# Performance work log

Hardware: AMD Instinct MI355X
Metric: run time of the kernel (lower is better)

The kernel has to match this reference:

```python
import jax, jax.numpy as jnp
import numpy as np


def setup_inputs() -> dict:
    key = jax.random.key(0)
    ks = jax.random.split(key, 5)
    B, C, H, W = 4, 512, 64, 64
    A = 64  # attention_features
    s = lambda fan_in: 1.0 / np.sqrt(fan_in)
    return {
        "x": jax.random.normal(ks[0], (B, C, H, W), dtype=jnp.float32),
        "Wf": jax.random.normal(ks[1], (C, A), dtype=jnp.float32) * s(C),
        "bf": jnp.zeros((A,), dtype=jnp.float32),
        "Wg": jax.random.normal(ks[2], (C, A), dtype=jnp.float32) * s(C),
        "bg": jnp.zeros((A,), dtype=jnp.float32),
        "Wh": jax.random.normal(ks[3], (C, C), dtype=jnp.float32) * s(C),
        "bh": jnp.zeros((C,), dtype=jnp.float32),
        "scale": jax.random.uniform(ks[4], (), dtype=jnp.float32),
    }


def reference(x, Wf, bf, Wg, bg, Wh, bh, scale):
    B, C, H, W = x.shape
    N = H * W

    def conv1x1(w, b):  # 1x1 conv == per-pixel matmul over channels
        return jnp.einsum('bchw,cf->bfhw', x, w) + b[None, :, None, None]

    f = conv1x1(Wf, bf)  # [B, A, H, W]
    g = conv1x1(Wg, bg)  # [B, A, H, W]
    h = conv1x1(Wh, bh)  # [B, C, H, W]

    # flatten_hw (channels_first): [B, C', H, W] -> [B, N, C']
    flat = lambda t: t.reshape(B, t.shape[1], N).transpose(0, 2, 1)
    gf = flat(g)  # [B, N, A]
    ff = flat(f)  # [B, N, A]
    hf = flat(h)  # [B, N, C]

    s = jnp.einsum('bnd,bmd->bnm', gf, ff)       # [B, N, N]
    attn = jax.nn.softmax(s, axis=-1)
    o = jnp.einsum('bnm,bmc->bnc', attn, hf)     # [B, N, C]
    # Original does a raw reshape back to x's shape (no transpose) — keep it.
    y = scale * o.reshape(x.shape) + x
    return y
```

## Files before the change

kernel.cpp:

```cpp
#include <hip/hip_runtime.h>
#include <hip/hip_bf16.h>

constexpr int BB = 4;
constexpr int C  = 512;
constexpr int A  = 64;
constexpr int N  = 4096;

typedef __attribute__((ext_vector_type(8))) short s16x8;
typedef __attribute__((ext_vector_type(4))) float f32x4;

#define MFMA_16x16x32_BF16(a, b, c) __builtin_amdgcn_mfma_f32_16x16x32_bf16((a), (b), (c), 0, 0, 0)

typedef __attribute__((address_space(3))) unsigned int lds_u32_t;
typedef const __attribute__((address_space(1))) unsigned int glb_u32_t;

__device__ __forceinline__ void gl2lds16(const void* g, void* l) {
    __builtin_amdgcn_global_load_lds((glb_u32_t*)g, (lds_u32_t*)l, 16, 0, 0);
}

#define GLOAD(dst, base, off)                                                  \
    asm volatile("global_load_dwordx4 %0, %1, %2"                              \
                 : "=v"(dst) : "v"(off), "s"(base))

__global__ __launch_bounds__(256) void k_trans(const float* __restrict__ src,
                                               __hip_bfloat16* __restrict__ dst,
                                               int K, int M) {
    __shared__ __hip_bfloat16 Ls[64][66];
    int m0 = blockIdx.x << 6, k0 = blockIdx.y << 6;
    size_t bo = (size_t)blockIdx.z * K * M;
    int t = threadIdx.x;
    int lm = t & 63, g = t >> 6;
    #pragma unroll
    for (int j = 0; j < 16; ++j) {
        int kk = j * 4 + g;
        Ls[kk][lm] = __float2bfloat16(src[bo + (size_t)(k0 + kk) * M + m0 + lm]);
    }
    __syncthreads();
    #pragma unroll
    for (int j = 0; j < 16; ++j) {
        int mm = j * 4 + g;
        dst[bo + (size_t)(m0 + mm) * K + k0 + lm] = Ls[lm][mm];
    }
}

__global__ __launch_bounds__(256) void k_trans2(const float* __restrict__ src,
                                                __hip_bfloat16* __restrict__ dhi,
                                                __hip_bfloat16* __restrict__ dlo,
                                                int K, int M) {
    __shared__ float Ls[64][65];
    int m0 = blockIdx.x << 6, k0 = blockIdx.y << 6;
    size_t bo = (size_t)blockIdx.z * K * M;
    int t = threadIdx.x;
    int lm = t & 63, g = t >> 6;
    #pragma unroll
    for (int j = 0; j < 16; ++j) {
        int kk = j * 4 + g;
        Ls[kk][lm] = src[bo + (size_t)(k0 + kk) * M + m0 + lm];
    }
    __syncthreads();
    #pragma unroll
    for (int j = 0; j < 16; ++j) {
        int mm = j * 4 + g;
        float v = Ls[lm][mm];
        __hip_bfloat16 h = __float2bfloat16(v);
        size_t idx = bo + (size_t)(m0 + mm) * K + k0 + lm;
        dhi[idx] = h;
        dlo[idx] = __float2bfloat16(v - __bfloat162float(h));
    }
}

__global__ __launch_bounds__(256) void k_fgm(const __hip_bfloat16* __restrict__ XThi, const __hip_bfloat16* __restrict__ XTlo,
                                             const __hip_bfloat16* __restrict__ WfThi, const __hip_bfloat16* __restrict__ WfTlo,
                                             const __hip_bfloat16* __restrict__ WgThi, const __hip_bfloat16* __restrict__ WgTlo,
                                             const float* __restrict__ bfv, const float* __restrict__ bgv,
                                             __hip_bfloat16* __restrict__ FFhi, __hip_bfloat16* __restrict__ FFlo,
                                             __hip_bfloat16* __restrict__ GFhi, __hip_bfloat16* __restrict__ GFlo) {
    __shared__ __align__(16) __hip_bfloat16 Ah[64 * 32], Al[64 * 32];
    __shared__ __align__(16) __hip_bfloat16 Bh[128 * 32], Bl[128 * 32];
    int r0 = blockIdx.x << 6;
    int t = threadIdx.x;
    int w = t >> 6, l = t & 63;
    int ln15 = l & 15, quad = l >> 4;
    int mh = w & 1, nh = w >> 1;

    f32x4 acc[2][4];
    #pragma unroll
    for (int mi = 0; mi < 2; ++mi)
        #pragma unroll
        for (int ni = 0; ni < 4; ++ni) acc[mi][ni] = (f32x4){0.f, 0.f, 0.f, 0.f};

    for (int kt = 0; kt < C; kt += 32) {
        {
            int row = t >> 2, seg = t & 3;
            int gseg = (seg - (row >> 1)) & 3;
            size_t go = (size_t)(r0 + row) * C + kt + gseg * 8;
            gl2lds16(XThi + go, &Ah[t * 8]);
            gl2lds16(XTlo + go, &Al[t * 8]);
        }
        #pragma unroll
        for (int j = 0; j < 2; ++j) {
            int i = j * 256 + t;
            int row = i >> 2, seg = i & 3;
            int gseg = (seg - (row >> 1)) & 3;
            size_t go = (size_t)(row & 63) * C + kt + gseg * 8;
            const __hip_bfloat16* bh = j ? WgThi : WfThi;
            const __hip_bfloat16* bl = j ? WgTlo : WfTlo;
            gl2lds16(bh + go, &Bh[i * 8]);
            gl2lds16(bl + go, &Bl[i * 8]);
        }
        __syncthreads();
        s16x8 afh[2], afl[2], bfh[4], bfl[4];
        #pragma unroll
        for (int mi = 0; mi < 2; ++mi) {
            int row = mh * 32 + mi * 16 + ln15;
            int sw = ((quad + (row >> 1)) & 3) << 3;
            afh[mi] = *(const s16x8*)&Ah[row * 32 + sw];
            afl[mi] = *(const s16x8*)&Al[row * 32 + sw];
        }
        #pragma unroll
        for (int ni = 0; ni < 4; ++ni) {
            int row = nh * 64 + ni * 16 + ln15;
            int sw = ((quad + (row >> 1)) & 3) << 3;
            bfh[ni] = *(const s16x8*)&Bh[row * 32 + sw];
            bfl[ni] = *(const s16x8*)&Bl[row * 32 + sw];
        }
        #pragma unroll
        for (int mi = 0; mi < 2; ++mi)
            #pragma unroll
            for (int ni = 0; ni < 4; ++ni) {
                acc[mi][ni] = MFMA_16x16x32_BF16(afh[mi], bfh[ni], acc[mi][ni]);
                acc[mi][ni] = MFMA_16x16x32_BF16(afl[mi], bfh[ni], acc[mi][ni]);
                acc[mi][ni] = MFMA_16x16x32_BF16(afh[mi], bfl[ni], acc[mi][ni]);
            }
        __syncthreads();
    }

    #pragma unroll
    for (int mi = 0; mi < 2; ++mi) {
        #pragma unroll
        for (int r = 0; r < 4; ++r) {
            size_t grow = (size_t)(r0 + mh * 32 + mi * 16 + quad * 4 + r) * A;
            #pragma unroll
            for (int ni = 0; ni < 4; ++ni) {
                int col = nh * 64 + ni * 16 + ln15;
                if (col < A) {
                    float v = acc[mi][ni][r] + bfv[col];
                    __hip_bfloat16 h = __float2bfloat16(v);
                    FFhi[grow + col] = h;
                    FFlo[grow + col] = __float2bfloat16(v - __bfloat162float(h));
                } else {
                    int a = col - A;
                    float v = acc[mi][ni][r] + bgv[a];
                    __hip_bfloat16 h = __float2bfloat16(v);
                    GFhi[grow + a] = h;
                    GFlo[grow + a] = __float2bfloat16(v - __bfloat162float(h));
                }
            }
        }
    }
}

__global__ __launch_bounds__(256) void k_hm(const __hip_bfloat16* __restrict__ WhT,
                                            const __hip_bfloat16* __restrict__ XT,
                                            const float* __restrict__ bhv,
                                            __hip_bfloat16* __restrict__ HFT) {
    __shared__ __align__(16) __hip_bfloat16 As[128 * 32];
    __shared__ __align__(16) __hip_bfloat16 Bs[128 * 32];
    int b  = blockIdx.z;
    int c0 = blockIdx.x << 7;
    int n0 = blockIdx.y << 7;
    int t = threadIdx.x;
    int w = t >> 6, l = t & 63;
    int ln15 = l & 15, quad = l >> 4;
    int mc = (w >> 1) << 6, nn = (w & 1) << 6;

    const __hip_bfloat16* Bb = XT + (size_t)b * N * C;

    f32x4 acc[4][4];
    #pragma unroll
    for (int mi = 0; mi < 4; ++mi)
        #pragma unroll
        for (int ni = 0; ni < 4; ++ni) acc[mi][ni] = (f32x4){0.f, 0.f, 0.f, 0.f};

    for (int kt = 0; kt < C; kt += 32) {
        #pragma unroll
        for (int j = 0; j < 2; ++j) {
            int i = j * 256 + t;
            int row = i >> 2, seg = i & 3;
            int gseg = (seg - (row >> 1)) & 3;
            gl2lds16(WhT + ((size_t)(c0 + row) * C + kt + gseg * 8), &As[i * 8]);
        }
        #pragma unroll
        for (int j = 0; j < 2; ++j) {
            int i = j * 256 + t;
            int row = i >> 2, seg = i & 3;
            int gseg = (seg - (row >> 1)) & 3;
            gl2lds16(Bb + ((size_t)(n0 + row) * C + kt + gseg * 8), &Bs[i * 8]);
        }
        __syncthreads();
        s16x8 af[4], bf2[4];
        #pragma unroll
        for (int mi = 0; mi < 4; ++mi) {
            int row = mc + mi * 16 + ln15;
            int sw = ((quad + (row >> 1)) & 3) << 3;
            af[mi] = *(const s16x8*)&As[row * 32 + sw];
        }
        #pragma unroll
        for (int ni = 0; ni < 4; ++ni) {
            int row = nn + ni * 16 + ln15;
            int sw = ((quad + (row >> 1)) & 3) << 3;
            bf2[ni] = *(const s16x8*)&Bs[row * 32 + sw];
        }
        #pragma unroll
        for (int mi = 0; mi < 4; ++mi)
            #pragma unroll
            for (int ni = 0; ni < 4; ++ni)
                acc[mi][ni] = MFMA_16x16x32_BF16(af[mi], bf2[ni], acc[mi][ni]);
        __syncthreads();
    }

    #pragma unroll
    for (int mi = 0; mi < 4; ++mi) {
        #pragma unroll
        for (int r = 0; r < 4; ++r) {
            int c = c0 + mc + mi * 16 + quad * 4 + r;
            float bias = bhv[c];
            size_t rowbase = ((size_t)b * C + c) * N;
            #pragma unroll
            for (int ni = 0; ni < 4; ++ni) {
                int n = n0 + nn + ni * 16 + ln15;
                HFT[rowbase + n] = __float2bfloat16(acc[mi][ni][r] + bias);
            }
        }
    }
}

__global__ __launch_bounds__(512, 2) void k_so(const __hip_bfloat16* __restrict__ GFhi, const __hip_bfloat16* __restrict__ GFlo,
                                               const __hip_bfloat16* __restrict__ FFhi, const __hip_bfloat16* __restrict__ FFlo,
                                               const __hip_bfloat16* __restrict__ HFT,
                                               const float* __restrict__ x,
                                               const float* __restrict__ scalep,
                                               float* __restrict__ out) {
    __shared__ __align__(16) __hip_bfloat16 Pl[2][64 * 64];
    __shared__ float sred[8][32];
    __shared__ float rsum[64];

    int id  = blockIdx.x;
    int xcd = id & 7;
    int b   = xcd >> 1;
    int qs  = ((id >> 3) << 1) | (xcd & 1);
    int q0  = qs << 6;

    int t = threadIdx.x;
    int w = t >> 6, l = t & 63;
    int ln15 = l & 15, quad = l >> 4, q8 = quad << 3;
    int qh = w >> 2, kq = w & 3;

    const __hip_bfloat16* Fh = FFhi + (size_t)b * N * A;
    const __hip_bfloat16* Fl = FFlo + (size_t)b * N * A;
    const __hip_bfloat16* Hb = HFT  + (size_t)b * C * N;

    s16x8 ah[2][2], al[2][2];
    #pragma unroll
    for (int mi = 0; mi < 2; ++mi) {
        const __hip_bfloat16* gp = GFhi + (size_t)(b * N + q0 + qh * 32 + mi * 16 + ln15) * A + q8;
        const __hip_bfloat16* lp = GFlo + (size_t)(b * N + q0 + qh * 32 + mi * 16 + ln15) * A + q8;
        ah[mi][0] = *(const s16x8*)gp; ah[mi][1] = *(const s16x8*)(gp + 32);
        al[mi][0] = *(const s16x8*)lp; al[mi][1] = *(const s16x8*)(lp + 32);
    }

    f32x4 acc[4][4];
    #pragma unroll
    for (int mi = 0; mi < 4; ++mi)
        #pragma unroll
        for (int ni = 0; ni < 4; ++ni) acc[mi][ni] = (f32x4){0.f, 0.f, 0.f, 0.f};
    float sm[2][4] = {{0.f,0.f,0.f,0.f},{0.f,0.f,0.f,0.f}};

    uint32_t hoffb[4];
    #pragma unroll
    for (int ni = 0; ni < 4; ++ni)
        hoffb[ni] = (uint32_t)((((w * 64 + ni * 16 + ln15) * N) + q8) * 2);
    uint32_t foff = (uint32_t)(((kq * 16 + ln15) * A + q8) * 2);
    int key2 = (kq * 16 + ln15) << 1;

    s16x8 hA[8], hB[8], fA[4], fB[4];
    #pragma unroll
    for (int ni = 0; ni < 4; ++ni) {
        GLOAD(hA[ni],     Hb, hoffb[ni]);
        GLOAD(hA[4 + ni], Hb, hoffb[ni] + 64u);
    }
    GLOAD(fA[0], Fh, foff);
    GLOAD(fA[1], Fh, foff + 64u);
    GLOAD(fA[2], Fl, foff);
    GLOAD(fA[3], Fl, foff + 64u);

#define KITER(KT, PBUF, HC, FC, HN, FN)                                        \
    {                                                                          \
        int ktn = ((KT) + 64) & (N - 1);     \
        uint32_t ktn2 = (uint32_t)(ktn << 1);                                  \
        uint32_t ktnf = (uint32_t)(ktn << 7);                                  \
        _Pragma("unroll")                                                      \
        for (int ni = 0; ni < 4; ++ni) {                                       \
            GLOAD(HN[ni],     Hb, hoffb[ni] + ktn2);                           \
            GLOAD(HN[4 + ni], Hb, hoffb[ni] + ktn2 + 64u);                     \
        }                                                                      \
        GLOAD(FN[0], Fh, foff + ktnf);                                         \
        GLOAD(FN[1], Fh, foff + ktnf + 64u);                                   \
        GLOAD(FN[2], Fl, foff + ktnf);                                         \
        GLOAD(FN[3], Fl, foff + ktnf + 64u);                                   \
        asm volatile("s_waitcnt vmcnt(12)" ::: "memory");                      \
        __builtin_amdgcn_sched_barrier(0);                                     \
        _Pragma("unroll")                                                      \
        for (int mi = 0; mi < 2; ++mi) {                                       \
            f32x4 s = {0.f, 0.f, 0.f, 0.f};                                    \
            s = MFMA_16x16x32_BF16(ah[mi][0], FC[0], s);                       \
            s = MFMA_16x16x32_BF16(ah[mi][1], FC[1], s);                       \
            s = MFMA_16x16x32_BF16(al[mi][0], FC[0], s);                       \
            s = MFMA_16x16x32_BF16(al[mi][1], FC[1], s);                       \
            s = MFMA_16x16x32_BF16(ah[mi][0], FC[2], s);                       \
            s = MFMA_16x16x32_BF16(ah[mi][1], FC[3], s);                       \
            _Pragma("unroll")                                                  \
            for (int r = 0; r < 4; ++r) {                                      \
                int q = qh * 32 + mi * 16 + quad * 4 + r;                      \
                float p = __expf(s[r]);         \
                __hip_bfloat16 pb = __float2bfloat16(p);                       \
                sm[mi][r] += __bfloat162float(pb);                             \
                *(__hip_bfloat16*)((char*)(PBUF) + q * 128 + (key2 ^ ((q & 7) << 4))) = pb; \
            }                                                                  \
        }                                                                      \
        asm volatile("s_waitcnt lgkmcnt(0)" ::: "memory");                     \
        __builtin_amdgcn_sched_barrier(0);                                     \
        __builtin_amdgcn_s_barrier();         \
        _Pragma("unroll")                                                      \
        for (int ks = 0; ks < 2; ++ks) {                                       \
            s16x8 pa[4];                                                       \
            _Pragma("unroll")                                                  \
            for (int mi = 0; mi < 4; ++mi) {                                   \
                int q = mi * 16 + ln15;                                        \
                pa[mi] = *(const s16x8*)((char*)(PBUF) + q * 128 + ((ks * 64 + quad * 16) ^ ((q & 7) << 4))); \
            }                                                                  \
            _Pragma("unroll")                                                  \
            for (int mi = 0; mi < 4; ++mi)                                     \
                _Pragma("unroll")                                              \
                for (int ni = 0; ni < 4; ++ni)                                 \
                    acc[mi][ni] = MFMA_16x16x32_BF16(pa[mi], HC[ks * 4 + ni], acc[mi][ni]); \
        }                                                                      \
    }

    for (int kt = 0; kt < N; kt += 128) {
        KITER(kt,      (&Pl[0][0]), hA, fA, hB, fB);
        KITER(kt + 64, (&Pl[1][0]), hB, fB, hA, fA);
    }
#undef KITER

    #pragma unroll
    for (int mi = 0; mi < 2; ++mi)
        #pragma unroll
        for (int r = 0; r < 4; ++r)
            #pragma unroll
            for (int d = 1; d < 16; d <<= 1)
                sm[mi][r] += __shfl_xor(sm[mi][r], d, 64);
    if (ln15 == 0) {
        #pragma unroll
        for (int mi = 0; mi < 2; ++mi)
            #pragma unroll
            for (int r = 0; r < 4; ++r)
                sred[w][mi * 16 + quad * 4 + r] = sm[mi][r];
    }
    __syncthreads();
    if (t < 64) {
        int base = (t >> 5) << 2, ix = t & 31;
        rsum[t] = sred[base][ix] + sred[base + 1][ix] + sred[base + 2][ix] + sred[base + 3][ix];
    }
    __syncthreads();

    float scv = *scalep;
    #pragma unroll
    for (int mi = 0; mi < 4; ++mi) {
        #pragma unroll
        for (int r = 0; r < 4; ++r) {
            int q = mi * 16 + quad * 4 + r;
            float srs = scv / rsum[q];
            size_t rowbase = (size_t)(b * N + q0 + q) * C;
            #pragma unroll
            for (int ni = 0; ni < 4; ++ni) {
                size_t idx = rowbase + w * 64 + ni * 16 + ln15;
                out[idx] = acc[mi][ni][r] * srs + x[idx];
            }
        }
    }
}

extern "C" void kernel_launch(void* const* d_in, const int* in_sizes, int n_in,
                              void* d_out, int out_size, void* d_ws, size_t ws_size,
                              hipStream_t stream) {
    const float* x   = (const float*)d_in[0];
    const float* Wf  = (const float*)d_in[1];
    const float* bfv = (const float*)d_in[2];
    const float* Wg  = (const float*)d_in[3];
    const float* bgv = (const float*)d_in[4];
    const float* Wh  = (const float*)d_in[5];
    const float* bhv = (const float*)d_in[6];
    const float* sc  = (const float*)d_in[7];
    float* out = (float*)d_out;

    char* ws = (char*)d_ws;
    size_t off = 0;
    __hip_bfloat16* FFhi = (__hip_bfloat16*)(ws + off); off += (size_t)BB * N * A * 2;
    __hip_bfloat16* FFlo = (__hip_bfloat16*)(ws + off); off += (size_t)BB * N * A * 2;
    __hip_bfloat16* GFhi = (__hip_bfloat16*)(ws + off); off += (size_t)BB * N * A * 2;
    __hip_bfloat16* GFlo = (__hip_bfloat16*)(ws + off); off += (size_t)BB * N * A * 2;
    __hip_bfloat16* HFT  = (__hip_bfloat16*)(ws + off); off += (size_t)BB * C * N * 2;
    char* Pbase          = (ws + off);                  off += (size_t)BB * N * N * 2;
    off += (size_t)BB * N * 4;
    __hip_bfloat16* WhT  = (__hip_bfloat16*)(ws + off); off += (size_t)C * C * 2;
    __hip_bfloat16* WfThi = (__hip_bfloat16*)(ws + off); off += (size_t)A * C * 2;
    __hip_bfloat16* WfTlo = (__hip_bfloat16*)(ws + off); off += (size_t)A * C * 2;
    __hip_bfloat16* WgThi = (__hip_bfloat16*)(ws + off); off += (size_t)A * C * 2;
    __hip_bfloat16* WgTlo = (__hip_bfloat16*)(ws + off); off += (size_t)A * C * 2;
    __hip_bfloat16* XThi = (__hip_bfloat16*)(Pbase + (size_t)BB * N * N * 2 - (size_t)BB * N * C * 2);
    __hip_bfloat16* XTlo = (__hip_bfloat16*)(Pbase + (size_t)BB * N * N * 2 - 2 * (size_t)BB * N * C * 2);

    k_trans<<<dim3(C / 64, C / 64, 1), dim3(256), 0, stream>>>(Wh, WhT, C, C);
    k_trans2<<<dim3(N / 64, C / 64, BB), dim3(256), 0, stream>>>(x, XThi, XTlo, C, N);
    k_trans2<<<dim3(A / 64, C / 64, 1), dim3(256), 0, stream>>>(Wf, WfThi, WfTlo, C, A);
    k_trans2<<<dim3(A / 64, C / 64, 1), dim3(256), 0, stream>>>(Wg, WgThi, WgTlo, C, A);
    k_hm<<<dim3(C / 128, N / 128, BB), dim3(256), 0, stream>>>(WhT, XThi, bhv, HFT);
    k_fgm<<<dim3((BB * N) / 64), dim3(256), 0, stream>>>(XThi, XTlo, WfThi, WfTlo, WgThi, WgTlo,
                                                         bfv, bgv, FFhi, FFlo, GFhi, GFlo);
    k_so<<<dim3(BB * (N / 64)), dim3(512), 0, stream>>>(GFhi, GFlo, FFhi, FFlo, HFT, x, sc, out);
}
```

Measured before the change: 346.9 us.

## Stage H tiles into LDS via async global-to-LDS loads with double buffering

The H operand of the attention-times-values MFMA is now loaded from global memory straight into a double-buffered LDS tile with swizzled layout, instead of directly into registers. The P buffer shrinks to a single buffer, with an extra barrier at the end of each iteration to protect it. Wave priority raising (s_setprio) is added around the MFMA sections. This frees VGPRs and may give better-coalesced H loads, but the kernel now needs about 136KB of LDS per block, so two 512-thread blocks can no longer share a CU. It also adds a barrier per iteration.

```diff
diff --git a/kernel.cpp b/kernel.cpp
--- a/kernel.cpp
+++ b/kernel.cpp
@@ -241,7 +241,8 @@
                                                const float* __restrict__ x,
                                                const float* __restrict__ scalep,
                                                float* __restrict__ out) {
-    __shared__ __align__(16) __hip_bfloat16 Pl[2][64 * 64];
+    __shared__ __align__(16) __hip_bfloat16 Hs[2][C * 64];
+    __shared__ __align__(16) __hip_bfloat16 Pl[64 * 64];
     __shared__ float sred[8][32];
     __shared__ float rsum[64];
 
@@ -255,6 +256,7 @@
     int w = t >> 6, l = t & 63;
     int ln15 = l & 15, quad = l >> 4, q8 = quad << 3;
     int qh = w >> 2, kq = w & 3;
+    int lr = l >> 3, ls = l & 7;
 
     const __hip_bfloat16* Fh = FFhi + (size_t)b * N * A;
     const __hip_bfloat16* Fl = FFlo + (size_t)b * N * A;
@@ -276,40 +278,31 @@
         for (int ni = 0; ni < 4; ++ni) acc[mi][ni] = (f32x4){0.f, 0.f, 0.f, 0.f};
     float sm[2][4] = {{0.f,0.f,0.f,0.f},{0.f,0.f,0.f,0.f}};
 
-    uint32_t hoffb[4];
-    #pragma unroll
-    for (int ni = 0; ni < 4; ++ni)
-        hoffb[ni] = (uint32_t)((((w * 64 + ni * 16 + ln15) * N) + q8) * 2);
+    const __hip_bfloat16* hsrc0 = Hb + (size_t)(w * 8 + lr) * N + ((ls ^ lr) << 3);
     uint32_t foff = (uint32_t)(((kq * 16 + ln15) * A + q8) * 2);
     int key2 = (kq * 16 + ln15) << 1;
 
-    s16x8 hA[8], hB[8], fA[4], fB[4];
-    #pragma unroll
-    for (int ni = 0; ni < 4; ++ni) {
-        GLOAD(hA[ni],     Hb, hoffb[ni]);
-        GLOAD(hA[4 + ni], Hb, hoffb[ni] + 64u);
-    }
-    GLOAD(fA[0], Fh, foff);
-    GLOAD(fA[1], Fh, foff + 64u);
-    GLOAD(fA[2], Fl, foff);
-    GLOAD(fA[3], Fl, foff + 64u);
-
-#define KITER(KT, PBUF, HC, FC, HN, FN)                                        \
+#define STAGE_H(BUF, KT)                                                       \
+    _Pragma("unroll")                                                          \
+    for (int r = 0; r < 8; ++r)                                                \
+        gl2lds16(hsrc0 + (size_t)(r * 64) * N + (KT),                          \
+                 &Hs[BUF][(r * 64 + w * 8) * 64]);
+
+    s16x8 fA[4], fB[4];
+    STAGE_H(0, 0)
+    GLOAD(fA[0], Fh, foff);        GLOAD(fA[1], Fh, foff + 64u);
+    GLOAD(fA[2], Fl, foff);        GLOAD(fA[3], Fl, foff + 64u);
+
+#define KITER(KT, BUF, FC, FN)                                                 \
     {                                                                          \
         int ktn = ((KT) + 64) & (N - 1);     \
-        uint32_t ktn2 = (uint32_t)(ktn << 1);                                  \
         uint32_t ktnf = (uint32_t)(ktn << 7);                                  \
-        _Pragma("unroll")                                                      \
-        for (int ni = 0; ni < 4; ++ni) {                                       \
-            GLOAD(HN[ni],     Hb, hoffb[ni] + ktn2);                           \
-            GLOAD(HN[4 + ni], Hb, hoffb[ni] + ktn2 + 64u);                     \
-        }                                                                      \
-        GLOAD(FN[0], Fh, foff + ktnf);                                         \
-        GLOAD(FN[1], Fh, foff + ktnf + 64u);                                   \
-        GLOAD(FN[2], Fl, foff + ktnf);                                         \
-        GLOAD(FN[3], Fl, foff + ktnf + 64u);                                   \
+        STAGE_H(BUF ^ 1, ktn)                                                  \
+        GLOAD(FN[0], Fh, foff + ktnf); GLOAD(FN[1], Fh, foff + ktnf + 64u);    \
+        GLOAD(FN[2], Fl, foff + ktnf); GLOAD(FN[3], Fl, foff + ktnf + 64u);    \
         asm volatile("s_waitcnt vmcnt(12)" ::: "memory");                      \
         __builtin_amdgcn_sched_barrier(0);                                     \
+        __builtin_amdgcn_s_setprio(1);                                         \
         _Pragma("unroll")                                                      \
         for (int mi = 0; mi < 2; ++mi) {                                       \
             f32x4 s = {0.f, 0.f, 0.f, 0.f};                                    \
@@ -325,33 +318,44 @@
                 float p = __expf(s[r]);         \
                 __hip_bfloat16 pb = __float2bfloat16(p);                       \
                 sm[mi][r] += __bfloat162float(pb);                             \
-                *(__hip_bfloat16*)((char*)(PBUF) + q * 128 + (key2 ^ ((q & 7) << 4))) = pb; \
+                *(__hip_bfloat16*)((char*)Pl + q * 128 + (key2 ^ ((q & 7) << 4))) = pb; \
             }                                                                  \
         }                                                                      \
+        __builtin_amdgcn_s_setprio(0);                                         \
         asm volatile("s_waitcnt lgkmcnt(0)" ::: "memory");                     \
         __builtin_amdgcn_sched_barrier(0);                                     \
-        __builtin_amdgcn_s_barrier();         \
+        __builtin_amdgcn_s_barrier();      \
+        __builtin_amdgcn_s_setprio(1);                                         \
         _Pragma("unroll")                                                      \
         for (int ks = 0; ks < 2; ++ks) {                                       \
-            s16x8 pa[4];                                                       \
+            s16x8 pa[4], hf[4];                                                \
             _Pragma("unroll")                                                  \
             for (int mi = 0; mi < 4; ++mi) {                                   \
                 int q = mi * 16 + ln15;                                        \
-                pa[mi] = *(const s16x8*)((char*)(PBUF) + q * 128 + ((ks * 64 + quad * 16) ^ ((q & 7) << 4))); \
+                pa[mi] = *(const s16x8*)((char*)Pl + q * 128 + ((ks * 64 + quad * 16) ^ ((q & 7) << 4))); \
+            }                                                                  \
+            _Pragma("unroll")                                                  \
+            for (int ni = 0; ni < 4; ++ni) {                                   \
+                int c = w * 64 + ni * 16 + ln15;                               \
+                hf[ni] = *(const s16x8*)((char*)&Hs[BUF][0] + c * 128 + (((ks * 4 + quad) ^ (ln15 & 7)) << 4)); \
             }                                                                  \
             _Pragma("unroll")                                                  \
             for (int mi = 0; mi < 4; ++mi)                                     \
                 _Pragma("unroll")                                              \
                 for (int ni = 0; ni < 4; ++ni)                                 \
-                    acc[mi][ni] = MFMA_16x16x32_BF16(pa[mi], HC[ks * 4 + ni], acc[mi][ni]); \
+                    acc[mi][ni] = MFMA_16x16x32_BF16(pa[mi], hf[ni], acc[mi][ni]); \
         }                                                                      \
+        __builtin_amdgcn_s_setprio(0);                                         \
+        __builtin_amdgcn_sched_barrier(0);                                     \
+        __builtin_amdgcn_s_barrier();          \
     }
 
     for (int kt = 0; kt < N; kt += 128) {
-        KITER(kt,      (&Pl[0][0]), hA, fA, hB, fB);
-        KITER(kt + 64, (&Pl[1][0]), hB, fB, hA, fA);
+        KITER(kt,      0, fA, fB)
+        KITER(kt + 64, 1, fB, fA)
     }
 #undef KITER
+#undef STAGE_H
 
     #pragma unroll
     for (int mi = 0; mi < 2; ++mi)
```

After: 284.1 us. -18.1%, faster.
